# Performance work log

Hardware: AMD Instinct MI355X
Metric: run time of the kernel (lower is better)

## Reference

```python
import jax, jax.numpy as jnp
import numpy as np

D_MODEL = 256
NHEAD = 4
HEAD_DIM = D_MODEL // NHEAD
EPS = 1e-5


def layernorm(x, g, b):
    mu = jnp.mean(x, axis=-1, keepdims=True)
    var = jnp.mean((x - mu) ** 2, axis=-1, keepdims=True)
    return (x - mu) * jax.lax.rsqrt(var + EPS) * g + b


def setup_inputs() -> dict:
    key = jax.random.key(0)
    ks = jax.random.split(key, 16)
    bs, L, S = 2, 2048, 2048
    inp = {
        "x": jax.random.normal(ks[0], (bs, L, D_MODEL), jnp.float32),
        "source": jax.random.normal(ks[1], (bs, S, D_MODEL), jnp.float32),
        "x_pe": jax.random.normal(ks[2], (bs, L, D_MODEL), jnp.float32),
        "source_pe": jax.random.normal(ks[3], (bs, S, D_MODEL), jnp.float32),
        "x_mask": jax.random.randint(ks[4], (bs, L), 0, 2).astype(bool),
        "source_mask": jax.random.randint(ks[5], (bs, S), 0, 2).astype(bool),
        "compatibility": jax.random.uniform(ks[6], (bs, L, S), jnp.float32),
        # learned params (bias-free linears, two layernorms)
        "Wq": jax.random.normal(ks[7], (D_MODEL, D_MODEL), jnp.float32) * 0.05,
        "Wk": jax.random.normal(ks[8], (D_MODEL, D_MODEL), jnp.float32) * 0.05,
        "Wv": jax.random.normal(ks[9], (D_MODEL, D_MODEL), jnp.float32) * 0.05,
        "Wmerge": jax.random.normal(ks[10], (D_MODEL, D_MODEL), jnp.float32) * 0.05,
        "Wmlp1": jax.random.normal(ks[11], (2 * D_MODEL, 2 * D_MODEL), jnp.float32) * 0.05,
        "Wmlp2": jax.random.normal(ks[12], (2 * D_MODEL, D_MODEL), jnp.float32) * 0.05,
        "ln1_g": jnp.ones((D_MODEL,), jnp.float32),
        "ln1_b": jnp.zeros((D_MODEL,), jnp.float32),
        "ln2_g": jnp.ones((D_MODEL,), jnp.float32),
        "ln2_b": jnp.zeros((D_MODEL,), jnp.float32),
    }
    return inp


def reference(x, source, x_pe, source_pe, x_mask, source_mask, compatibility,
              Wq, Wk, Wv, Wmerge, Wmlp1, Wmlp2, ln1_g, ln1_b, ln2_g, ln2_b):
    bs = x.shape[0]
    # pe_type == 'sinusoidal': add PE before projections
    q_in = x + x_pe
    k_in = source + source_pe
    qw = (q_in @ Wq).reshape(bs, -1, NHEAD, HEAD_DIM)
    kw = (k_in @ Wk).reshape(bs, -1, NHEAD, HEAD_DIM)
    vw = (source @ Wv).reshape(bs, -1, NHEAD, HEAD_DIM)
    # scores (n, l, s, h)
    a = jnp.einsum('nlhd,nshd->nlsh', qw, kw)
    a = a * compatibility[..., None]
    mask = x_mask[:, :, None, None] & (~source_mask)[:, None, :, None]
    a = jnp.where(mask, -jnp.inf, a)
    a = a / jnp.sqrt(jnp.asarray(HEAD_DIM, a.dtype))
    a = jax.nn.softmax(a, axis=2)
    o = jnp.einsum('nlsh,nshd->nlhd', a, vw).reshape(bs, -1, D_MODEL)
    message = layernorm(o @ Wmerge, ln1_g, ln1_b)
    h = jnp.concatenate([x, message], axis=2)
    message = jax.nn.relu(h @ Wmlp1) @ Wmlp2
    message = layernorm(message, ln2_g, ln2_b)
    return x + message
```

## Files before the change

### kernel.cpp

```cpp
#include <hip/hip_runtime.h>
#include <cstddef>
#include <math.h>

#define D_MODEL 256
#define NHEAD 4
#define HEAD_DIM 64
#define BSZ 2
#define SEQ 2048
#define MROWS (BSZ * SEQ)
#define NSPLIT 4
#define SCHUNK (SEQ / NSPLIT)

typedef __attribute__((ext_vector_type(8))) short short8;
typedef __attribute__((ext_vector_type(4))) float f32x4;

__device__ __forceinline__ ushort f2bf_bits(float f) {
    union { float f; unsigned u; } c; c.f = f;
    unsigned u = c.u + 0x7fffu + ((c.u >> 16) & 1u);
    return (ushort)(u >> 16);
}
__device__ __forceinline__ float bf2f(ushort u) {
    union { unsigned u; float f; } c; c.u = (unsigned)u << 16;
    return c.f;
}

__global__ __launch_bounds__(256) void prepw_k(
    const float* __restrict__ Wq, const float* __restrict__ Wk,
    const float* __restrict__ Wv, const float* __restrict__ Wm,
    const float* __restrict__ W1, const float* __restrict__ W2,
    ushort* __restrict__ Wqt, ushort* __restrict__ Wkt,
    ushort* __restrict__ Wvt, ushort* __restrict__ Wmt,
    ushort* __restrict__ W1t, ushort* __restrict__ W2t)
{
    const int f0 = (blockIdx.x * 256 + threadIdx.x) * 16;
    const float* in; ushort* out; int Nd, ksh, r;
    if (f0 < 262144) {
        const int w = f0 >> 16; r = f0 & 65535; Nd = 256; ksh = 8;
        in  = (w == 0) ? Wq  : (w == 1) ? Wk  : (w == 2) ? Wv  : Wm;
        out = (w == 0) ? Wqt : (w == 1) ? Wkt : (w == 2) ? Wvt : Wmt;
    } else if (f0 < 524288) { r = f0 - 262144; Nd = 512; ksh = 9; in = W1; out = W1t; }
    else                    { r = f0 - 524288; Nd = 256; ksh = 9; in = W2; out = W2t; }
    const int n = r >> ksh, k = r & ((1 << ksh) - 1);
    ushort tmp[16];
#pragma unroll
    for (int i = 0; i < 16; i++) tmp[i] = f2bf_bits(in[(size_t)(k + i) * Nd + n]);
    *(uint4*)&out[r]     = *(uint4*)&tmp[0];
    *(uint4*)&out[r + 8] = *(uint4*)&tmp[8];
}

__global__ __launch_bounds__(256) void qkvp_k(
    const float* __restrict__ x, const float* __restrict__ xpe,
    const float* __restrict__ src, const float* __restrict__ spe,
    const ushort* __restrict__ Wqt, const ushort* __restrict__ Wkt,
    const ushort* __restrict__ Wvt,
    ushort* __restrict__ Qb, ushort* __restrict__ Kb, ushort* __restrict__ VtG)
{
    __shared__ __attribute__((aligned(16))) ushort As[16][264];

    const int z = blockIdx.y;
    const float* A1 = (z == 0) ? x : src;
    const float* A2 = (z == 0) ? xpe : (z == 1) ? spe : nullptr;
    const ushort* Bt = (z == 0) ? Wqt : (z == 1) ? Wkt : Wvt;
    ushort* out      = (z == 0) ? Qb  : (z == 1) ? Kb  : VtG;

    const int t = threadIdx.x, w = t >> 6, lane = t & 63;
    const int quad = lane >> 4, l16 = lane & 15;
    const int row0 = blockIdx.x * 16;

    {
        const int r = t >> 4, c0 = (t & 15) * 16;
        const size_t base = (size_t)(row0 + r) * 256 + c0;
        ushort tmp[16];
#pragma unroll
        for (int i = 0; i < 16; i += 4) {
            float4 a = *(const float4*)&A1[base + i];
            if (z < 2) {
                const float4 p = *(const float4*)&A2[base + i];
                a.x += p.x; a.y += p.y; a.z += p.z; a.w += p.w;
            }
            tmp[i] = f2bf_bits(a.x); tmp[i + 1] = f2bf_bits(a.y);
            tmp[i + 2] = f2bf_bits(a.z); tmp[i + 3] = f2bf_bits(a.w);
        }
        *(uint4*)&As[r][c0]     = *(uint4*)&tmp[0];
        *(uint4*)&As[r][c0 + 8] = *(uint4*)&tmp[8];
    }
    __syncthreads();

    f32x4 acc[4] = {};
#pragma unroll
    for (int k0 = 0; k0 < 256; k0 += 32) {
        const short8 aq = *(const short8*)&As[l16][k0 + quad * 8];
#pragma unroll
        for (int ct = 0; ct < 4; ct++) {
            const short8 bk =
                *(const short8*)&Bt[(size_t)(w * 64 + ct * 16 + l16) * 256 + k0 + quad * 8];
            acc[ct] = __builtin_amdgcn_mfma_f32_16x16x32_bf16(aq, bk, acc[ct], 0, 0, 0);
        }
    }

#pragma unroll
    for (int ct = 0; ct < 4; ct++) {
#pragma unroll
        for (int reg = 0; reg < 4; reg++) {
            const int grow = row0 + quad * 4 + reg;
            const int col  = w * 64 + ct * 16 + l16;
            const ushort v = f2bf_bits(acc[ct][reg]);
            if (z < 2) {
                out[(size_t)grow * 256 + col] = v;
            } else {
                const int b = grow >> 11, s = grow & 2047;
                out[((size_t)(b * 256 + col)) * 2048 + s] = v;
            }
        }
    }
}

__global__ __launch_bounds__(256, 4) void attn_k(
    const ushort* __restrict__ Q, const ushort* __restrict__ K,
    const ushort* __restrict__ Vt, const float* __restrict__ comp,
    const int* __restrict__ xmask, const int* __restrict__ smask,
    ushort* __restrict__ Opart, float* __restrict__ lbuf)
{
    __shared__ __attribute__((aligned(16))) ushort Ks[64][72];
    __shared__ __attribute__((aligned(16))) ushort Vs[64][72];
    __shared__ __attribute__((aligned(16))) ushort Ps[64][72];
    __shared__ int xms[64];
    __shared__ int sms[64];

    const int t    = threadIdx.x;
    const int w    = t >> 6;
    const int lane = t & 63;
    const int quad = lane >> 4;
    const int l16  = lane & 15;
    const int l0   = blockIdx.x * 64;
    const int h    = blockIdx.y;
    const int b    = blockIdx.z >> 2;
    const int sc   = blockIdx.z & 3;
    const int sbeg = sc * SCHUNK;

    const ushort* qp =
        &Q[((size_t)(b * SEQ + l0 + w * 16 + l16)) * D_MODEL + h * HEAD_DIM + quad * 8];
    const short8 q0 = *(const short8*)qp;
    const short8 q1 = *(const short8*)(qp + 32);

    if (t < 64) xms[t] = xmask[b * SEQ + l0 + t];

    const int rowbase = w * 16 + quad * 4;
    const int arow    = w * 16 + l16;
    const float* crow = comp + ((size_t)b * SEQ + l0 + rowbase) * SEQ;

    float lpart[4] = {0.f, 0.f, 0.f, 0.f};
    f32x4 oacc[4] = {};

    for (int s0 = sbeg; s0 < sbeg + SCHUNK; s0 += 64) {
        __syncthreads();
#pragma unroll
        for (int i = 0; i < 2; i++) {
            const int e = t + i * 256, r = e >> 3, cg = (e & 7) * 8;
            *(uint4*)&Ks[r][cg] =
                *(const uint4*)&K[((size_t)(b * SEQ + s0 + r)) * D_MODEL + h * HEAD_DIM + cg];
            *(uint4*)&Vs[r][cg] =
                *(const uint4*)&Vt[((size_t)(b * 256 + h * HEAD_DIM + r)) * SEQ + s0 + cg];
        }
        if (t < 64) sms[t] = smask[b * SEQ + s0 + t];

        float cv[16];
#pragma unroll
        for (int reg = 0; reg < 4; reg++)
#pragma unroll
            for (int ct = 0; ct < 4; ct++)
                cv[reg * 4 + ct] = crow[(size_t)reg * SEQ + s0 + ct * 16 + l16];

        __syncthreads();

        f32x4 sacc[4] = {};
#pragma unroll
        for (int ct = 0; ct < 4; ct++) {
            const short8 bk0 = *(const short8*)&Ks[ct * 16 + l16][quad * 8];
            sacc[ct] = __builtin_amdgcn_mfma_f32_16x16x32_bf16(q0, bk0, sacc[ct], 0, 0, 0);
        }
#pragma unroll
        for (int ct = 0; ct < 4; ct++) {
            const short8 bk1 = *(const short8*)&Ks[ct * 16 + l16][32 + quad * 8];
            sacc[ct] = __builtin_amdgcn_mfma_f32_16x16x32_bf16(q1, bk1, sacc[ct], 0, 0, 0);
        }

        const int sm0 = sms[l16], sm1 = sms[16 + l16], sm2 = sms[32 + l16], sm3 = sms[48 + l16];
#pragma unroll
        for (int reg = 0; reg < 4; reg++) {
            const bool xm = (xms[rowbase + reg] != 0);
            const float p0 = (xm && sm0 == 0) ? 0.f : __expf(sacc[0][reg] * cv[reg * 4 + 0] * 0.125f);
            const float p1 = (xm && sm1 == 0) ? 0.f : __expf(sacc[1][reg] * cv[reg * 4 + 1] * 0.125f);
            const float p2 = (xm && sm2 == 0) ? 0.f : __expf(sacc[2][reg] * cv[reg * 4 + 2] * 0.125f);
            const float p3 = (xm && sm3 == 0) ? 0.f : __expf(sacc[3][reg] * cv[reg * 4 + 3] * 0.125f);
            lpart[reg] += p0 + p1 + p2 + p3;
            Ps[rowbase + reg][l16]      = f2bf_bits(p0);
            Ps[rowbase + reg][16 + l16] = f2bf_bits(p1);
            Ps[rowbase + reg][32 + l16] = f2bf_bits(p2);
            Ps[rowbase + reg][48 + l16] = f2bf_bits(p3);
        }

#pragma unroll
        for (int kc = 0; kc < 64; kc += 32) {
            const short8 ap = *(const short8*)&Ps[arow][kc + quad * 8];
#pragma unroll
            for (int ct = 0; ct < 4; ct++) {
                const short8 bv = *(const short8*)&Vs[ct * 16 + l16][kc + quad * 8];
                oacc[ct] = __builtin_amdgcn_mfma_f32_16x16x32_bf16(ap, bv, oacc[ct], 0, 0, 0);
            }
        }
    }

#pragma unroll
    for (int off = 1; off < 16; off <<= 1)
#pragma unroll
        for (int reg = 0; reg < 4; reg++)
            lpart[reg] += __shfl_xor(lpart[reg], off, 64);

#pragma unroll
    for (int ct = 0; ct < 4; ct++)
#pragma unroll
        for (int reg = 0; reg < 4; reg++) {
            const int grow = b * SEQ + l0 + rowbase + reg;
            Opart[((size_t)sc * MROWS + grow) * D_MODEL + h * HEAD_DIM + ct * 16 + l16] =
                f2bf_bits(oacc[ct][reg]);
        }
    if (l16 == 0) {
#pragma unroll
        for (int reg = 0; reg < 4; reg++) {
            const int grow = b * SEQ + l0 + rowbase + reg;
            lbuf[((size_t)(sc * NHEAD + h)) * MROWS + grow] = lpart[reg];
        }
    }
}

__global__ __launch_bounds__(256) void tail_k(
    const ushort* __restrict__ Opart, const float* __restrict__ lbuf,
    const ushort* __restrict__ Wmt, const ushort* __restrict__ W1t,
    const ushort* __restrict__ W2t,
    const float* __restrict__ g1, const float* __restrict__ b1,
    const float* __restrict__ g2, const float* __restrict__ b2,
    const float* __restrict__ x, float* __restrict__ out)
{
    __shared__ __attribute__((aligned(16))) ushort As[16][264];
    __shared__ __attribute__((aligned(16))) ushort AH[16][520];
    __shared__ __attribute__((aligned(16))) ushort Hs[16][520];
    __shared__ float redS[4][16], redQ[4][16];

    const int t = threadIdx.x, w = t >> 6, lane = t & 63;
    const int quad = lane >> 4, l16 = lane & 15;
    const int row0 = blockIdx.x * 16;

    {
        const int r = t >> 4, cg = (t & 15) * 16;
        const int grow = row0 + r, h = (t & 15) >> 2;
        ushort tmp[16];
#pragma unroll
        for (int i = 0; i < 16; i += 4) {
            const float4 a = *(const float4*)&x[(size_t)grow * 256 + cg + i];
            tmp[i] = f2bf_bits(a.x); tmp[i + 1] = f2bf_bits(a.y);
            tmp[i + 2] = f2bf_bits(a.z); tmp[i + 3] = f2bf_bits(a.w);
        }
        *(uint4*)&AH[r][cg]     = *(uint4*)&tmp[0];
        *(uint4*)&AH[r][cg + 8] = *(uint4*)&tmp[8];

        float den = 0.f;
        float num[16] = {};
#pragma unroll
        for (int c = 0; c < NSPLIT; c++) {
            den += lbuf[((size_t)(c * NHEAD + h)) * MROWS + grow];
            const ushort* p = &Opart[((size_t)c * MROWS + grow) * D_MODEL + cg];
            uint4 u0 = *(const uint4*)p, u1 = *(const uint4*)(p + 8);
            const ushort* us0 = (const ushort*)&u0;
            const ushort* us1 = (const ushort*)&u1;
#pragma unroll
            for (int i = 0; i < 8; i++) { num[i] += bf2f(us0[i]); num[8 + i] += bf2f(us1[i]); }
        }
        const float inv = 1.f / den;
#pragma unroll
        for (int i = 0; i < 16; i++) tmp[i] = f2bf_bits(num[i] * inv);
        *(uint4*)&As[r][cg]     = *(uint4*)&tmp[0];
        *(uint4*)&As[r][cg + 8] = *(uint4*)&tmp[8];
    }
    __syncthreads();

    f32x4 macc[4] = {};
#pragma unroll
    for (int k0 = 0; k0 < 256; k0 += 32) {
        const short8 aq = *(const short8*)&As[l16][k0 + quad * 8];
#pragma unroll
        for (int ct = 0; ct < 4; ct++) {
            const short8 bk =
                *(const short8*)&Wmt[(size_t)(w * 64 + ct * 16 + l16) * 256 + k0 + quad * 8];
            macc[ct] = __builtin_amdgcn_mfma_f32_16x16x32_bf16(aq, bk, macc[ct], 0, 0, 0);
        }
    }

    {
        float ps[4] = {}, pq[4] = {};
#pragma unroll
        for (int ct = 0; ct < 4; ct++)
#pragma unroll
            for (int reg = 0; reg < 4; reg++) {
                ps[reg] += macc[ct][reg];
                pq[reg] += macc[ct][reg] * macc[ct][reg];
            }
#pragma unroll
        for (int off = 1; off < 16; off <<= 1)
#pragma unroll
            for (int reg = 0; reg < 4; reg++) {
                ps[reg] += __shfl_xor(ps[reg], off, 64);
                pq[reg] += __shfl_xor(pq[reg], off, 64);
            }
        if (l16 == 0)
#pragma unroll
            for (int reg = 0; reg < 4; reg++) {
                redS[w][quad * 4 + reg] = ps[reg];
                redQ[w][quad * 4 + reg] = pq[reg];
            }
    }
    __syncthreads();

#pragma unroll
    for (int reg = 0; reg < 4; reg++) {
        const int lrow = quad * 4 + reg;
        const float s  = redS[0][lrow] + redS[1][lrow] + redS[2][lrow] + redS[3][lrow];
        const float s2 = redQ[0][lrow] + redQ[1][lrow] + redQ[2][lrow] + redQ[3][lrow];
        const float mu  = s * (1.f / 256.f);
        const float var = s2 * (1.f / 256.f) - mu * mu;
        const float rr  = rsqrtf(var + 1e-5f);
#pragma unroll
        for (int ct = 0; ct < 4; ct++) {
            const int col = w * 64 + ct * 16 + l16;
            AH[lrow][256 + col] = f2bf_bits((macc[ct][reg] - mu) * rr * g1[col] + b1[col]);
        }
    }
    __syncthreads();

    {
        f32x4 hacc[8] = {};
#pragma unroll
        for (int k0 = 0; k0 < 512; k0 += 32) {
            const short8 aq = *(const short8*)&AH[l16][k0 + quad * 8];
#pragma unroll
            for (int ct = 0; ct < 8; ct++) {
                const short8 bk =
                    *(const short8*)&W1t[(size_t)(w * 128 + ct * 16 + l16) * 512 + k0 + quad * 8];
                hacc[ct] = __builtin_amdgcn_mfma_f32_16x16x32_bf16(aq, bk, hacc[ct], 0, 0, 0);
            }
        }
#pragma unroll
        for (int ct = 0; ct < 8; ct++)
#pragma unroll
            for (int reg = 0; reg < 4; reg++)
                Hs[quad * 4 + reg][w * 128 + ct * 16 + l16] =
                    f2bf_bits(fmaxf(hacc[ct][reg], 0.f));
    }
    __syncthreads();

    f32x4 acc[4] = {};
#pragma unroll
    for (int k0 = 0; k0 < 512; k0 += 32) {
        const short8 ap = *(const short8*)&Hs[l16][k0 + quad * 8];
#pragma unroll
        for (int ct = 0; ct < 4; ct++) {
            const short8 bk =
                *(const short8*)&W2t[(size_t)(w * 64 + ct * 16 + l16) * 512 + k0 + quad * 8];
            acc[ct] = __builtin_amdgcn_mfma_f32_16x16x32_bf16(ap, bk, acc[ct], 0, 0, 0);
        }
    }

    {
        float ps[4] = {}, pq[4] = {};
#pragma unroll
        for (int ct = 0; ct < 4; ct++)
#pragma unroll
            for (int reg = 0; reg < 4; reg++) {
                ps[reg] += acc[ct][reg];
                pq[reg] += acc[ct][reg] * acc[ct][reg];
            }
#pragma unroll
        for (int off = 1; off < 16; off <<= 1)
#pragma unroll
            for (int reg = 0; reg < 4; reg++) {
                ps[reg] += __shfl_xor(ps[reg], off, 64);
                pq[reg] += __shfl_xor(pq[reg], off, 64);
            }
        if (l16 == 0)
#pragma unroll
            for (int reg = 0; reg < 4; reg++) {
                redS[w][quad * 4 + reg] = ps[reg];
                redQ[w][quad * 4 + reg] = pq[reg];
            }
    }
    __syncthreads();

#pragma unroll
    for (int reg = 0; reg < 4; reg++) {
        const int lrow = quad * 4 + reg;
        const float s  = redS[0][lrow] + redS[1][lrow] + redS[2][lrow] + redS[3][lrow];
        const float s2 = redQ[0][lrow] + redQ[1][lrow] + redQ[2][lrow] + redQ[3][lrow];
        const float mu  = s * (1.f / 256.f);
        const float var = s2 * (1.f / 256.f) - mu * mu;
        const float rr  = rsqrtf(var + 1e-5f);
#pragma unroll
        for (int ct = 0; ct < 4; ct++) {
            const int col = w * 64 + ct * 16 + l16;
            const size_t idx = (size_t)(row0 + lrow) * 256 + col;
            out[idx] = (acc[ct][reg] - mu) * rr * g2[col] + b2[col] + x[idx];
        }
    }
}

extern "C" void kernel_launch(void* const* d_in, const int* in_sizes, int n_in,
                              void* d_out, int out_size, void* d_ws, size_t ws_size,
                              hipStream_t stream)
{
    (void)in_sizes; (void)n_in; (void)out_size; (void)ws_size;
    const float* x      = (const float*)d_in[0];
    const float* source = (const float*)d_in[1];
    const float* x_pe   = (const float*)d_in[2];
    const float* s_pe   = (const float*)d_in[3];
    const int*   x_mask = (const int*)d_in[4];
    const int*   s_mask = (const int*)d_in[5];
    const float* comp   = (const float*)d_in[6];
    const float* Wq     = (const float*)d_in[7];
    const float* Wk     = (const float*)d_in[8];
    const float* Wv     = (const float*)d_in[9];
    const float* Wmerge = (const float*)d_in[10];
    const float* Wmlp1  = (const float*)d_in[11];
    const float* Wmlp2  = (const float*)d_in[12];
    const float* ln1_g  = (const float*)d_in[13];
    const float* ln1_b  = (const float*)d_in[14];
    const float* ln2_g  = (const float*)d_in[15];
    const float* ln2_b  = (const float*)d_in[16];
    float* out = (float*)d_out;
    char*  ws  = (char*)d_ws;

    const size_t MB = 1024 * 1024;
    ushort* Qb    = (ushort*)(ws + 0 * MB);
    ushort* Kb    = (ushort*)(ws + 2 * MB);
    ushort* VtG   = (ushort*)(ws + 4 * MB);
    ushort* Opart = (ushort*)(ws + 6 * MB);
    float*  lbuf  = (float*)(ws + 14 * MB);
    ushort* Wqt   = (ushort*)(ws + 15 * MB);
    ushort* Wkt   = (ushort*)(ws + 15 * MB + 128 * 1024);
    ushort* Wvt   = (ushort*)(ws + 15 * MB + 256 * 1024);
    ushort* Wmt   = (ushort*)(ws + 15 * MB + 384 * 1024);
    ushort* W1t   = (ushort*)(ws + 15 * MB + 512 * 1024);
    ushort* W2t   = (ushort*)(ws + 16 * MB);

    prepw_k<<<160, 256, 0, stream>>>(Wq, Wk, Wv, Wmerge, Wmlp1, Wmlp2,
                                     Wqt, Wkt, Wvt, Wmt, W1t, W2t);

    qkvp_k<<<dim3(MROWS / 16, 3), 256, 0, stream>>>(
        x, x_pe, source, s_pe, Wqt, Wkt, Wvt, Qb, Kb, VtG);

    attn_k<<<dim3(SEQ / 64, NHEAD, BSZ * NSPLIT), 256, 0, stream>>>(
        Qb, Kb, VtG, comp, x_mask, s_mask, Opart, lbuf);

    tail_k<<<MROWS / 16, 256, 0, stream>>>(
        Opart, lbuf, Wmt, W1t, W2t, ln1_g, ln1_b, ln2_g, ln2_b, x, out);
}
```

Measured before the change: 185.9 us.

## Fuse four kernels into one persistent kernel with grid-wide barriers

Merges the weight-prep, QKV projection, attention and tail kernels into a single launch of 1024 blocks that step through the phases, separated by atomic-counter grid barriers. Shared memory is a union of the per-phase layouts. The aim is to remove per-kernel launch overhead and the gaps between dependent launches. In exchange it adds a memset launch, spin-wait barriers that idle many blocks in the phases that use fewer blocks, and a deadlock risk if all 1024 blocks cannot be resident at once (256 CUs × 4 blocks).

Result: slower. 689.9 us (+271.1%).

```diff
diff --git a/kernel.cpp b/kernel.cpp
--- a/kernel.cpp
+++ b/kernel.cpp
@@ -10,6 +10,7 @@
 #define MROWS (BSZ * SEQ)
 #define NSPLIT 4
 #define SCHUNK (SEQ / NSPLIT)
+#define GRIDN 1024
 
 typedef __attribute__((ext_vector_type(8))) short short8;
 typedef __attribute__((ext_vector_type(4))) float f32x4;
@@ -24,390 +25,398 @@
     return c.f;
 }
 
-__global__ __launch_bounds__(256) void prepw_k(
-    const float* __restrict__ Wq, const float* __restrict__ Wk,
-    const float* __restrict__ Wv, const float* __restrict__ Wm,
-    const float* __restrict__ W1, const float* __restrict__ W2,
-    ushort* __restrict__ Wqt, ushort* __restrict__ Wkt,
-    ushort* __restrict__ Wvt, ushort* __restrict__ Wmt,
-    ushort* __restrict__ W1t, ushort* __restrict__ W2t)
-{
-    const int f0 = (blockIdx.x * 256 + threadIdx.x) * 16;
-    const float* in; ushort* out; int Nd, ksh, r;
-    if (f0 < 262144) {
-        const int w = f0 >> 16; r = f0 & 65535; Nd = 256; ksh = 8;
-        in  = (w == 0) ? Wq  : (w == 1) ? Wk  : (w == 2) ? Wv  : Wm;
-        out = (w == 0) ? Wqt : (w == 1) ? Wkt : (w == 2) ? Wvt : Wmt;
-    } else if (f0 < 524288) { r = f0 - 262144; Nd = 512; ksh = 9; in = W1; out = W1t; }
-    else                    { r = f0 - 524288; Nd = 256; ksh = 9; in = W2; out = W2t; }
-    const int n = r >> ksh, k = r & ((1 << ksh) - 1);
-    ushort tmp[16];
-#pragma unroll
-    for (int i = 0; i < 16; i++) tmp[i] = f2bf_bits(in[(size_t)(k + i) * Nd + n]);
-    *(uint4*)&out[r]     = *(uint4*)&tmp[0];
-    *(uint4*)&out[r + 8] = *(uint4*)&tmp[8];
-}
-
-__global__ __launch_bounds__(256) void qkvp_k(
-    const float* __restrict__ x, const float* __restrict__ xpe,
-    const float* __restrict__ src, const float* __restrict__ spe,
-    const ushort* __restrict__ Wqt, const ushort* __restrict__ Wkt,
-    const ushort* __restrict__ Wvt,
-    ushort* __restrict__ Qb, ushort* __restrict__ Kb, ushort* __restrict__ VtG)
-{
-    __shared__ __attribute__((aligned(16))) ushort As[16][264];
-
-    const int z = blockIdx.y;
-    const float* A1 = (z == 0) ? x : src;
-    const float* A2 = (z == 0) ? xpe : (z == 1) ? spe : nullptr;
-    const ushort* Bt = (z == 0) ? Wqt : (z == 1) ? Wkt : Wvt;
-    ushort* out      = (z == 0) ? Qb  : (z == 1) ? Kb  : VtG;
-
-    const int t = threadIdx.x, w = t >> 6, lane = t & 63;
-    const int quad = lane >> 4, l16 = lane & 15;
-    const int row0 = blockIdx.x * 16;
-
-    {
-        const int r = t >> 4, c0 = (t & 15) * 16;
-        const size_t base = (size_t)(row0 + r) * 256 + c0;
-        ushort tmp[16];
-#pragma unroll
-        for (int i = 0; i < 16; i += 4) {
-            float4 a = *(const float4*)&A1[base + i];
-            if (z < 2) {
-                const float4 p = *(const float4*)&A2[base + i];
-                a.x += p.x; a.y += p.y; a.z += p.z; a.w += p.w;
-            }
-            tmp[i] = f2bf_bits(a.x); tmp[i + 1] = f2bf_bits(a.y);
-            tmp[i + 2] = f2bf_bits(a.z); tmp[i + 3] = f2bf_bits(a.w);
-        }
-        *(uint4*)&As[r][c0]     = *(uint4*)&tmp[0];
-        *(uint4*)&As[r][c0 + 8] = *(uint4*)&tmp[8];
+struct Params {
+    const float *x, *xpe, *src, *spe;
+    const int *xmk, *smk;
+    const float *comp;
+    const float *Wq, *Wk, *Wv, *Wm, *W1, *W2;
+    const float *g1, *b1, *g2, *b2;
+    float *out;
+    ushort *Qb, *Kb, *VtG, *Opart;
+    float *lbuf;
+    ushort *Wqt, *Wkt, *Wvt, *Wmt, *W1t, *W2t;
+    int *bar;
+};
+
+__device__ __forceinline__ void gbar(int* ctr) {
+    __syncthreads();
+    __threadfence();
+    if (threadIdx.x == 0) {
+        atomicAdd(ctr, 1);
+        while (atomicAdd(ctr, 0) < GRIDN) __builtin_amdgcn_s_sleep(2);
     }
     __syncthreads();
-
-    f32x4 acc[4] = {};
-#pragma unroll
-    for (int k0 = 0; k0 < 256; k0 += 32) {
-        const short8 aq = *(const short8*)&As[l16][k0 + quad * 8];
+}
+
+struct SAttn {
+    ushort Ks[64][72];
+    ushort Vs[64][72];
+    ushort Ps[64][72];
+    int xms[64];
+    int sms[64];
+};
+struct STail {
+    ushort AH[16][520];
+    ushort Hs[16][520];
+    float redS[4][16];
+    float redQ[4][16];
+};
+struct SQkv { ushort As[16][264]; };
+union SMem { SAttn a; STail t; SQkv q; };
+
+__global__ __launch_bounds__(256, 4) void fused_k(Params p)
+{
+    __shared__ __attribute__((aligned(16))) SMem sm;
+
+    const int bid = blockIdx.x, t = threadIdx.x;
+    const int w = t >> 6, lane = t & 63;
+    const int quad = lane >> 4, l16 = lane & 15;
+
+    if (bid < 160) {
+        const int f0 = (bid * 256 + t) * 16;
+        const float* in; ushort* out; int Nd, ksh, r;
+        if (f0 < 262144) {
+            const int ws = f0 >> 16; r = f0 & 65535; Nd = 256; ksh = 8;
+            in  = (ws == 0) ? p.Wq  : (ws == 1) ? p.Wk  : (ws == 2) ? p.Wv  : p.Wm;
+            out = (ws == 0) ? p.Wqt : (ws == 1) ? p.Wkt : (ws == 2) ? p.Wvt : p.Wmt;
+        } else if (f0 < 524288) { r = f0 - 262144; Nd = 512; ksh = 9; in = p.W1; out = p.W1t; }
+        else                    { r = f0 - 524288; Nd = 256; ksh = 9; in = p.W2; out = p.W2t; }
+        const int n = r >> ksh, k = r & ((1 << ksh) - 1);
+        ushort tmp[16];
+#pragma unroll
+        for (int i = 0; i < 16; i++) tmp[i] = f2bf_bits(in[(size_t)(k + i) * Nd + n]);
+        *(uint4*)&out[r]     = *(uint4*)&tmp[0];
+        *(uint4*)&out[r + 8] = *(uint4*)&tmp[8];
+    }
+    gbar(&p.bar[0]);
+
+    if (bid < 768) {
+        const int z = bid >> 8;
+        const int row0 = (bid & 255) * 16;
+        const float* A1 = (z == 0) ? p.x : p.src;
+        const float* A2 = (z == 0) ? p.xpe : (z == 1) ? p.spe : nullptr;
+        const ushort* Bt = (z == 0) ? p.Wqt : (z == 1) ? p.Wkt : p.Wvt;
+        ushort* out      = (z == 0) ? p.Qb  : (z == 1) ? p.Kb  : p.VtG;
+
+        {
+            const int r = t >> 4, c0 = (t & 15) * 16;
+            const size_t base = (size_t)(row0 + r) * 256 + c0;
+            ushort tmp[16];
+#pragma unroll
+            for (int i = 0; i < 16; i += 4) {
+                float4 a = *(const float4*)&A1[base + i];
+                if (z < 2) {
+                    const float4 pe = *(const float4*)&A2[base + i];
+                    a.x += pe.x; a.y += pe.y; a.z += pe.z; a.w += pe.w;
+                }
+                tmp[i] = f2bf_bits(a.x); tmp[i + 1] = f2bf_bits(a.y);
+                tmp[i + 2] = f2bf_bits(a.z); tmp[i + 3] = f2bf_bits(a.w);
+            }
+            *(uint4*)&sm.q.As[r][c0]     = *(uint4*)&tmp[0];
+            *(uint4*)&sm.q.As[r][c0 + 8] = *(uint4*)&tmp[8];
+        }
+        __syncthreads();
+
+        f32x4 acc[4] = {};
+#pragma unroll
+        for (int k0 = 0; k0 < 256; k0 += 32) {
+            const short8 aq = *(const short8*)&sm.q.As[l16][k0 + quad * 8];
+#pragma unroll
+            for (int ct = 0; ct < 4; ct++) {
+                const short8 bk =
+                    *(const short8*)&Bt[(size_t)(w * 64 + ct * 16 + l16) * 256 + k0 + quad * 8];
+                acc[ct] = __builtin_amdgcn_mfma_f32_16x16x32_bf16(aq, bk, acc[ct], 0, 0, 0);
+            }
+        }
+
 #pragma unroll
         for (int ct = 0; ct < 4; ct++) {
-            const short8 bk =
-                *(const short8*)&Bt[(size_t)(w * 64 + ct * 16 + l16) * 256 + k0 + quad * 8];
-            acc[ct] = __builtin_amdgcn_mfma_f32_16x16x32_bf16(aq, bk, acc[ct], 0, 0, 0);
+#pragma unroll
+            for (int reg = 0; reg < 4; reg++) {
+                const int grow = row0 + quad * 4 + reg;
+                const int col  = w * 64 + ct * 16 + l16;
+                const ushort v = f2bf_bits(acc[ct][reg]);
+                if (z < 2) {
+                    out[(size_t)grow * 256 + col] = v;
+                } else {
+                    const int b = grow >> 11, s = grow & 2047;
+                    out[((size_t)(b * 256 + col)) * 2048 + s] = v;
+                }
+            }
         }
     }
-
-#pragma unroll
-    for (int ct = 0; ct < 4; ct++) {
+    gbar(&p.bar[1]);
+
+    {
+        const int l0 = (bid & 31) * 64;
+        const int h  = (bid >> 5) & 3;
+        const int zz = bid >> 7;
+        const int b  = zz >> 2;
+        const int sc = zz & 3;
+        const int sbeg = sc * SCHUNK;
+
+        const ushort* qp =
+            &p.Qb[((size_t)(b * SEQ + l0 + w * 16 + l16)) * D_MODEL + h * HEAD_DIM + quad * 8];
+        const short8 q0 = *(const short8*)qp;
+        const short8 q1 = *(const short8*)(qp + 32);
+
+        if (t < 64) sm.a.xms[t] = p.xmk[b * SEQ + l0 + t];
+
+        const int rowbase = w * 16 + quad * 4;
+        const int arow    = w * 16 + l16;
+        const float* crow = p.comp + ((size_t)b * SEQ + l0 + rowbase) * SEQ;
+
+        float lpart[4] = {0.f, 0.f, 0.f, 0.f};
+        f32x4 oacc[4] = {};
+
+        for (int s0 = sbeg; s0 < sbeg + SCHUNK; s0 += 64) {
+            __syncthreads();
+#pragma unroll
+            for (int i = 0; i < 2; i++) {
+                const int e = t + i * 256, r = e >> 3, cgc = (e & 7) * 8;
+                *(uint4*)&sm.a.Ks[r][cgc] =
+                    *(const uint4*)&p.Kb[((size_t)(b * SEQ + s0 + r)) * D_MODEL + h * HEAD_DIM + cgc];
+                *(uint4*)&sm.a.Vs[r][cgc] =
+                    *(const uint4*)&p.VtG[((size_t)(b * 256 + h * HEAD_DIM + r)) * SEQ + s0 + cgc];
+            }
+            if (t < 64) sm.a.sms[t] = p.smk[b * SEQ + s0 + t];
+
+            float cv[16];
+#pragma unroll
+            for (int reg = 0; reg < 4; reg++)
+#pragma unroll
+                for (int ct = 0; ct < 4; ct++)
+                    cv[reg * 4 + ct] = crow[(size_t)reg * SEQ + s0 + ct * 16 + l16];
+
+            __syncthreads();
+
+            f32x4 sacc[4] = {};
+#pragma unroll
+            for (int ct = 0; ct < 4; ct++) {
+                const short8 bk0 = *(const short8*)&sm.a.Ks[ct * 16 + l16][quad * 8];
+                sacc[ct] = __builtin_amdgcn_mfma_f32_16x16x32_bf16(q0, bk0, sacc[ct], 0, 0, 0);
+            }
+#pragma unroll
+            for (int ct = 0; ct < 4; ct++) {
+                const short8 bk1 = *(const short8*)&sm.a.Ks[ct * 16 + l16][32 + quad * 8];
+                sacc[ct] = __builtin_amdgcn_mfma_f32_16x16x32_bf16(q1, bk1, sacc[ct], 0, 0, 0);
+            }
+
+            const int s0m = sm.a.sms[l16], s1m = sm.a.sms[16 + l16];
+            const int s2m = sm.a.sms[32 + l16], s3m = sm.a.sms[48 + l16];
+#pragma unroll
+            for (int reg = 0; reg < 4; reg++) {
+                const bool xm = (sm.a.xms[rowbase + reg] != 0);
+                const float p0 = (xm && s0m == 0) ? 0.f : __expf(sacc[0][reg] * cv[reg * 4 + 0] * 0.125f);
+                const float p1 = (xm && s1m == 0) ? 0.f : __expf(sacc[1][reg] * cv[reg * 4 + 1] * 0.125f);
+                const float p2 = (xm && s2m == 0) ? 0.f : __expf(sacc[2][reg] * cv[reg * 4 + 2] * 0.125f);
+                const float p3 = (xm && s3m == 0) ? 0.f : __expf(sacc[3][reg] * cv[reg * 4 + 3] * 0.125f);
+                lpart[reg] += p0 + p1 + p2 + p3;
+                sm.a.Ps[rowbase + reg][l16]      = f2bf_bits(p0);
+                sm.a.Ps[rowbase + reg][16 + l16] = f2bf_bits(p1);
+                sm.a.Ps[rowbase + reg][32 + l16] = f2bf_bits(p2);
+                sm.a.Ps[rowbase + reg][48 + l16] = f2bf_bits(p3);
+            }
+
+#pragma unroll
+            for (int kc = 0; kc < 64; kc += 32) {
+                const short8 ap = *(const short8*)&sm.a.Ps[arow][kc + quad * 8];
+#pragma unroll
+                for (int ct = 0; ct < 4; ct++) {
+                    const short8 bv = *(const short8*)&sm.a.Vs[ct * 16 + l16][kc + quad * 8];
+                    oacc[ct] = __builtin_amdgcn_mfma_f32_16x16x32_bf16(ap, bv, oacc[ct], 0, 0, 0);
+                }
+            }
+        }
+
+#pragma unroll
+        for (int off = 1; off < 16; off <<= 1)
+#pragma unroll
+            for (int reg = 0; reg < 4; reg++)
+                lpart[reg] += __shfl_xor(lpart[reg], off, 64);
+
+#pragma unroll
+        for (int ct = 0; ct < 4; ct++)
+#pragma unroll
+            for (int reg = 0; reg < 4; reg++) {
+                const int grow = b * SEQ + l0 + rowbase + reg;
+                p.Opart[((size_t)sc * MROWS + grow) * D_MODEL + h * HEAD_DIM + ct * 16 + l16] =
+                    f2bf_bits(oacc[ct][reg]);
+            }
+        if (l16 == 0) {
+#pragma unroll
+            for (int reg = 0; reg < 4; reg++) {
+                const int grow = b * SEQ + l0 + rowbase + reg;
+                p.lbuf[((size_t)(sc * NHEAD + h)) * MROWS + grow] = lpart[reg];
+            }
+        }
+    }
+    gbar(&p.bar[2]);
+
+    if (bid < 256) {
+        const int row0 = bid * 16;
+        ushort* AsP = &sm.t.Hs[0][0];
+
+        {
+            const int r = t >> 4, cgc = (t & 15) * 16;
+            const int grow = row0 + r, h = (t & 15) >> 2;
+            ushort tmp[16];
+#pragma unroll
+            for (int i = 0; i < 16; i += 4) {
+                const float4 a = *(const float4*)&p.x[(size_t)grow * 256 + cgc + i];
+                tmp[i] = f2bf_bits(a.x); tmp[i + 1] = f2bf_bits(a.y);
+                tmp[i + 2] = f2bf_bits(a.z); tmp[i + 3] = f2bf_bits(a.w);
+            }
+            *(uint4*)&sm.t.AH[r][cgc]     = *(uint4*)&tmp[0];
+            *(uint4*)&sm.t.AH[r][cgc + 8] = *(uint4*)&tmp[8];
+
+            float den = 0.f;
+            float num[16] = {};
+#pragma unroll
+            for (int c = 0; c < NSPLIT; c++) {
+                den += p.lbuf[((size_t)(c * NHEAD + h)) * MROWS + grow];
+                const ushort* pp = &p.Opart[((size_t)c * MROWS + grow) * D_MODEL + cgc];
+                uint4 u0 = *(const uint4*)pp, u1 = *(const uint4*)(pp + 8);
+                const ushort* us0 = (const ushort*)&u0;
+                const ushort* us1 = (const ushort*)&u1;
+#pragma unroll
+                for (int i = 0; i < 8; i++) { num[i] += bf2f(us0[i]); num[8 + i] += bf2f(us1[i]); }
+            }
+            const float inv = 1.f / den;
+#pragma unroll
+            for (int i = 0; i < 16; i++) tmp[i] = f2bf_bits(num[i] * inv);
+            *(uint4*)&AsP[r * 264 + cgc]     = *(uint4*)&tmp[0];
+            *(uint4*)&AsP[r * 264 + cgc + 8] = *(uint4*)&tmp[8];
+        }
+        __syncthreads();
+
+        f32x4 macc[4] = {};
+#pragma unroll
+        for (int k0 = 0; k0 < 256; k0 += 32) {
+            const short8 aq = *(const short8*)&AsP[l16 * 264 + k0 + quad * 8];
+#pragma unroll
+            for (int ct = 0; ct < 4; ct++) {
+                const short8 bk =
+                    *(const short8*)&p.Wmt[(size_t)(w * 64 + ct * 16 + l16) * 256 + k0 + quad * 8];
+                macc[ct] = __builtin_amdgcn_mfma_f32_16x16x32_bf16(aq, bk, macc[ct], 0, 0, 0);
+            }
+        }
+
+        {
+            float ps[4] = {}, pq[4] = {};
+#pragma unroll
+            for (int ct = 0; ct < 4; ct++)
+#pragma unroll
+                for (int reg = 0; reg < 4; reg++) {
+                    ps[reg] += macc[ct][reg];
+                    pq[reg] += macc[ct][reg] * macc[ct][reg];
+                }
+#pragma unroll
+            for (int off = 1; off < 16; off <<= 1)
+#pragma unroll
+                for (int reg = 0; reg < 4; reg++) {
+                    ps[reg] += __shfl_xor(ps[reg], off, 64);
+                    pq[reg] += __shfl_xor(pq[reg], off, 64);
+                }
+            if (l16 == 0)
+#pragma unroll
+                for (int reg = 0; reg < 4; reg++) {
+                    sm.t.redS[w][quad * 4 + reg] = ps[reg];
+                    sm.t.redQ[w][quad * 4 + reg] = pq[reg];
+                }
+        }
+        __syncthreads();
+
 #pragma unroll
         for (int reg = 0; reg < 4; reg++) {
-            const int grow = row0 + quad * 4 + reg;
-            const int col  = w * 64 + ct * 16 + l16;
-            const ushort v = f2bf_bits(acc[ct][reg]);
-            if (z < 2) {
-                out[(size_t)grow * 256 + col] = v;
-            } else {
-                const int b = grow >> 11, s = grow & 2047;
-                out[((size_t)(b * 256 + col)) * 2048 + s] = v;
-            }
-        }
-    }
-}
-
-__global__ __launch_bounds__(256, 4) void attn_k(
-    const ushort* __restrict__ Q, const ushort* __restrict__ K,
-    const ushort* __restrict__ Vt, const float* __restrict__ comp,
-    const int* __restrict__ xmask, const int* __restrict__ smask,
-    ushort* __restrict__ Opart, float* __restrict__ lbuf)
-{
-    __shared__ __attribute__((aligned(16))) ushort Ks[64][72];
-    __shared__ __attribute__((aligned(16))) ushort Vs[64][72];
-    __shared__ __attribute__((aligned(16))) ushort Ps[64][72];
-    __shared__ int xms[64];
-    __shared__ int sms[64];
-
-    const int t    = threadIdx.x;
-    const int w    = t >> 6;
-    const int lane = t & 63;
-    const int quad = lane >> 4;
-    const int l16  = lane & 15;
-    const int l0   = blockIdx.x * 64;
-    const int h    = blockIdx.y;
-    const int b    = blockIdx.z >> 2;
-    const int sc   = blockIdx.z & 3;
-    const int sbeg = sc * SCHUNK;
-
-    const ushort* qp =
-        &Q[((size_t)(b * SEQ + l0 + w * 16 + l16)) * D_MODEL + h * HEAD_DIM + quad * 8];
-    const short8 q0 = *(const short8*)qp;
-    const short8 q1 = *(const short8*)(qp + 32);
-
-    if (t < 64) xms[t] = xmask[b * SEQ + l0 + t];
-
-    const int rowbase = w * 16 + quad * 4;
-    const int arow    = w * 16 + l16;
-    const float* crow = comp + ((size_t)b * SEQ + l0 + rowbase) * SEQ;
-
-    float lpart[4] = {0.f, 0.f, 0.f, 0.f};
-    f32x4 oacc[4] = {};
-
-    for (int s0 = sbeg; s0 < sbeg + SCHUNK; s0 += 64) {
-        __syncthreads();
-#pragma unroll
-        for (int i = 0; i < 2; i++) {
-            const int e = t + i * 256, r = e >> 3, cg = (e & 7) * 8;
-            *(uint4*)&Ks[r][cg] =
-                *(const uint4*)&K[((size_t)(b * SEQ + s0 + r)) * D_MODEL + h * HEAD_DIM + cg];
-            *(uint4*)&Vs[r][cg] =
-                *(const uint4*)&Vt[((size_t)(b * 256 + h * HEAD_DIM + r)) * SEQ + s0 + cg];
-        }
-        if (t < 64) sms[t] = smask[b * SEQ + s0 + t];
-
-        float cv[16];
-#pragma unroll
-        for (int reg = 0; reg < 4; reg++)
+            const int lrow = quad * 4 + reg;
+            const float s  = sm.t.redS[0][lrow] + sm.t.redS[1][lrow] + sm.t.redS[2][lrow] + sm.t.redS[3][lrow];
+            const float s2 = sm.t.redQ[0][lrow] + sm.t.redQ[1][lrow] + sm.t.redQ[2][lrow] + sm.t.redQ[3][lrow];
+            const float mu  = s * (1.f / 256.f);
+            const float var = s2 * (1.f / 256.f) - mu * mu;
+            const float rr  = rsqrtf(var + 1e-5f);
+#pragma unroll
+            for (int ct = 0; ct < 4; ct++) {
+                const int col = w * 64 + ct * 16 + l16;
+                sm.t.AH[lrow][256 + col] =
+                    f2bf_bits((macc[ct][reg] - mu) * rr * p.g1[col] + p.b1[col]);
+            }
+        }
+        __syncthreads();
+
+        {
+            f32x4 hacc[8] = {};
+#pragma unroll
+            for (int k0 = 0; k0 < 512; k0 += 32) {
+                const short8 aq = *(const short8*)&sm.t.AH[l16][k0 + quad * 8];
+#pragma unroll
+                for (int ct = 0; ct < 8; ct++) {
+                    const short8 bk =
+                        *(const short8*)&p.W1t[(size_t)(w * 128 + ct * 16 + l16) * 512 + k0 + quad * 8];
+                    hacc[ct] = __builtin_amdgcn_mfma_f32_16x16x32_bf16(aq, bk, hacc[ct], 0, 0, 0);
+                }
+            }
+            __syncthreads();
+#pragma unroll
+            for (int ct = 0; ct < 8; ct++)
+#pragma unroll
+                for (int reg = 0; reg < 4; reg++)
+                    sm.t.Hs[quad * 4 + reg][w * 128 + ct * 16 + l16] =
+                        f2bf_bits(fmaxf(hacc[ct][reg], 0.f));
+        }
+        __syncthreads();
+
+        f32x4 acc[4] = {};
+#pragma unroll
+        for (int k0 = 0; k0 < 512; k0 += 32) {
+            const short8 ap = *(const short8*)&sm.t.Hs[l16][k0 + quad * 8];
+#pragma unroll
+            for (int ct = 0; ct < 4; ct++) {
+                const short8 bk =
+                    *(const short8*)&p.W2t[(size_t)(w * 64 + ct * 16 + l16) * 512 + k0 + quad * 8];
+                acc[ct] = __builtin_amdgcn_mfma_f32_16x16x32_bf16(ap, bk, acc[ct], 0, 0, 0);
+            }
+        }
+
+        {
+            float ps[4] = {}, pq[4] = {};
 #pragma unroll
             for (int ct = 0; ct < 4; ct++)
-                cv[reg * 4 + ct] = crow[(size_t)reg * SEQ + s0 + ct * 16 + l16];
-
-        __syncthreads();
-
-        f32x4 sacc[4] = {};
-#pragma unroll
-        for (int ct = 0; ct < 4; ct++) {
-            const short8 bk0 = *(const short8*)&Ks[ct * 16 + l16][quad * 8];
-            sacc[ct] = __builtin_amdgcn_mfma_f32_16x16x32_bf16(q0, bk0, sacc[ct], 0, 0, 0);
-        }
-#pragma unroll
-        for (int ct = 0; ct < 4; ct++) {
-            const short8 bk1 = *(const short8*)&Ks[ct * 16 + l16][32 + quad * 8];
-            sacc[ct] = __builtin_amdgcn_mfma_f32_16x16x32_bf16(q1, bk1, sacc[ct], 0, 0, 0);
-        }
-
-        const int sm0 = sms[l16], sm1 = sms[16 + l16], sm2 = sms[32 + l16], sm3 = sms[48 + l16];
+#pragma unroll
+                for (int reg = 0; reg < 4; reg++) {
+                    ps[reg] += acc[ct][reg];
+                    pq[reg] += acc[ct][reg] * acc[ct][reg];
+                }
+#pragma unroll
+            for (int off = 1; off < 16; off <<= 1)
+#pragma unroll
+                for (int reg = 0; reg < 4; reg++) {
+                    ps[reg] += __shfl_xor(ps[reg], off, 64);
+                    pq[reg] += __shfl_xor(pq[reg], off, 64);
+                }
+            if (l16 == 0)
+#pragma unroll
+                for (int reg = 0; reg < 4; reg++) {
+                    sm.t.redS[w][quad * 4 + reg] = ps[reg];
+                    sm.t.redQ[w][quad * 4 + reg] = pq[reg];
+                }
+        }
+        __syncthreads();
+
 #pragma unroll
         for (int reg = 0; reg < 4; reg++) {
-            const bool xm = (xms[rowbase + reg] != 0);
-            const float p0 = (xm && sm0 == 0) ? 0.f : __expf(sacc[0][reg] * cv[reg * 4 + 0] * 0.125f);
-            const float p1 = (xm && sm1 == 0) ? 0.f : __expf(sacc[1][reg] * cv[reg * 4 + 1] * 0.125f);
-            const float p2 = (xm && sm2 == 0) ? 0.f : __expf(sacc[2][reg] * cv[reg * 4 + 2] * 0.125f);
-            const float p3 = (xm && sm3 == 0) ? 0.f : __expf(sacc[3][reg] * cv[reg * 4 + 3] * 0.125f);
-            lpart[reg] += p0 + p1 + p2 + p3;
-            Ps[rowbase + reg][l16]      = f2bf_bits(p0);
-            Ps[rowbase + reg][16 + l16] = f2bf_bits(p1);
-            Ps[rowbase + reg][32 + l16] = f2bf_bits(p2);
-            Ps[rowbase + reg][48 + l16] = f2bf_bits(p3);
-        }
-
-#pragma unroll
-        for (int kc = 0; kc < 64; kc += 32) {
-            const short8 ap = *(const short8*)&Ps[arow][kc + quad * 8];
-#pragma unroll
-            for (int ct = 0; ct < 4; ct++) {
-                const short8 bv = *(const short8*)&Vs[ct * 16 + l16][kc + quad * 8];
-                oacc[ct] = __builtin_amdgcn_mfma_f32_16x16x32_bf16(ap, bv, oacc[ct], 0, 0, 0);
-            }
-        }
-    }
-
-#pragma unroll
-    for (int off = 1; off < 16; off <<= 1)
-#pragma unroll
-        for (int reg = 0; reg < 4; reg++)
-            lpart[reg] += __shfl_xor(lpart[reg], off, 64);
-
-#pragma unroll
-    for (int ct = 0; ct < 4; ct++)
-#pragma unroll
-        for (int reg = 0; reg < 4; reg++) {
-            const int grow = b * SEQ + l0 + rowbase + reg;
-            Opart[((size_t)sc * MROWS + grow) * D_MODEL + h * HEAD_DIM + ct * 16 + l16] =
-                f2bf_bits(oacc[ct][reg]);
-        }
-    if (l16 == 0) {
-#pragma unroll
-        for (int reg = 0; reg < 4; reg++) {
-            const int grow = b * SEQ + l0 + rowbase + reg;
-            lbuf[((size_t)(sc * NHEAD + h)) * MROWS + grow] = lpart[reg];
-        }
-    }
-}
-
-__global__ __launch_bounds__(256) void tail_k(
-    const ushort* __restrict__ Opart, const float* __restrict__ lbuf,
-    const ushort* __restrict__ Wmt, const ushort* __restrict__ W1t,
-    const ushort* __restrict__ W2t,
-    const float* __restrict__ g1, const float* __restrict__ b1,
-    const float* __restrict__ g2, const float* __restrict__ b2,
-    const float* __restrict__ x, float* __restrict__ out)
-{
-    __shared__ __attribute__((aligned(16))) ushort As[16][264];
-    __shared__ __attribute__((aligned(16))) ushort AH[16][520];
-    __shared__ __attribute__((aligned(16))) ushort Hs[16][520];
-    __shared__ float redS[4][16], redQ[4][16];
-
-    const int t = threadIdx.x, w = t >> 6, lane = t & 63;
-    const int quad = lane >> 4, l16 = lane & 15;
-    const int row0 = blockIdx.x * 16;
-
-    {
-        const int r = t >> 4, cg = (t & 15) * 16;
-        const int grow = row0 + r, h = (t & 15) >> 2;
-        ushort tmp[16];
-#pragma unroll
-        for (int i = 0; i < 16; i += 4) {
-            const float4 a = *(const float4*)&x[(size_t)grow * 256 + cg + i];
-            tmp[i] = f2bf_bits(a.x); tmp[i + 1] = f2bf_bits(a.y);
-            tmp[i + 2] = f2bf_bits(a.z); tmp[i + 3] = f2bf_bits(a.w);
-        }
-        *(uint4*)&AH[r][cg]     = *(uint4*)&tmp[0];
-        *(uint4*)&AH[r][cg + 8] = *(uint4*)&tmp[8];
-
-        float den = 0.f;
-        float num[16] = {};
-#pragma unroll
-        for (int c = 0; c < NSPLIT; c++) {
-            den += lbuf[((size_t)(c * NHEAD + h)) * MROWS + grow];
-            const ushort* p = &Opart[((size_t)c * MROWS + grow) * D_MODEL + cg];
-            uint4 u0 = *(const uint4*)p, u1 = *(const uint4*)(p + 8);
-            const ushort* us0 = (const ushort*)&u0;
-            const ushort* us1 = (const ushort*)&u1;
-#pragma unroll
-            for (int i = 0; i < 8; i++) { num[i] += bf2f(us0[i]); num[8 + i] += bf2f(us1[i]); }
-        }
-        const float inv = 1.f / den;
-#pragma unroll
-        for (int i = 0; i < 16; i++) tmp[i] = f2bf_bits(num[i] * inv);
-        *(uint4*)&As[r][cg]     = *(uint4*)&tmp[0];
-        *(uint4*)&As[r][cg + 8] = *(uint4*)&tmp[8];
-    }
-    __syncthreads();
-
-    f32x4 macc[4] = {};
-#pragma unroll
-    for (int k0 = 0; k0 < 256; k0 += 32) {
-        const short8 aq = *(const short8*)&As[l16][k0 + quad * 8];
-#pragma unroll
-        for (int ct = 0; ct < 4; ct++) {
-            const short8 bk =
-                *(const short8*)&Wmt[(size_t)(w * 64 + ct * 16 + l16) * 256 + k0 + quad * 8];
-            macc[ct] = __builtin_amdgcn_mfma_f32_16x16x32_bf16(aq, bk, macc[ct], 0, 0, 0);
-        }
-    }
-
-    {
-        float ps[4] = {}, pq[4] = {};
-#pragma unroll
-        for (int ct = 0; ct < 4; ct++)
-#pragma unroll
-            for (int reg = 0; reg < 4; reg++) {
-                ps[reg] += macc[ct][reg];
-                pq[reg] += macc[ct][reg] * macc[ct][reg];
-            }
-#pragma unroll
-        for (int off = 1; off < 16; off <<= 1)
-#pragma unroll
-            for (int reg = 0; reg < 4; reg++) {
-                ps[reg] += __shfl_xor(ps[reg], off, 64);
-                pq[reg] += __shfl_xor(pq[reg], off, 64);
-            }
-        if (l16 == 0)
-#pragma unroll
-            for (int reg = 0; reg < 4; reg++) {
-                redS[w][quad * 4 + reg] = ps[reg];
-                redQ[w][quad * 4 + reg] = pq[reg];
-            }
-    }
-    __syncthreads();
-
-#pragma unroll
-    for (int reg = 0; reg < 4; reg++) {
-        const int lrow = quad * 4 + reg;
-        const float s  = redS[0][lrow] + redS[1][lrow] + redS[2][lrow] + redS[3][lrow];
-        const float s2 = redQ[0][lrow] + redQ[1][lrow] + redQ[2][lrow] + redQ[3][lrow];
-        const float mu  = s * (1.f / 256.f);
-        const float var = s2 * (1.f / 256.f) - mu * mu;
-        const float rr  = rsqrtf(var + 1e-5f);
-#pragma unroll
-        for (int ct = 0; ct < 4; ct++) {
-            const int col = w * 64 + ct * 16 + l16;
-            AH[lrow][256 + col] = f2bf_bits((macc[ct][reg] - mu) * rr * g1[col] + b1[col]);
-        }
-    }
-    __syncthreads();
-
-    {
-        f32x4 hacc[8] = {};
-#pragma unroll
-        for (int k0 = 0; k0 < 512; k0 += 32) {
-            const short8 aq = *(const short8*)&AH[l16][k0 + quad * 8];
-#pragma unroll
-            for (int ct = 0; ct < 8; ct++) {
-                const short8 bk =
-                    *(const short8*)&W1t[(size_t)(w * 128 + ct * 16 + l16) * 512 + k0 + quad * 8];
-                hacc[ct] = __builtin_amdgcn_mfma_f32_16x16x32_bf16(aq, bk, hacc[ct], 0, 0, 0);
-            }
-        }
-#pragma unroll
-        for (int ct = 0; ct < 8; ct++)
-#pragma unroll
-            for (int reg = 0; reg < 4; reg++)
-                Hs[quad * 4 + reg][w * 128 + ct * 16 + l16] =
-                    f2bf_bits(fmaxf(hacc[ct][reg], 0.f));
-    }
-    __syncthreads();
-
-    f32x4 acc[4] = {};
-#pragma unroll
-    for (int k0 = 0; k0 < 512; k0 += 32) {
-        const short8 ap = *(const short8*)&Hs[l16][k0 + quad * 8];
-#pragma unroll
-        for (int ct = 0; ct < 4; ct++) {
-            const short8 bk =
-                *(const short8*)&W2t[(size_t)(w * 64 + ct * 16 + l16) * 512 + k0 + quad * 8];
-            acc[ct] = __builtin_amdgcn_mfma_f32_16x16x32_bf16(ap, bk, acc[ct], 0, 0, 0);
-        }
-    }
-
-    {
-        float ps[4] = {}, pq[4] = {};
-#pragma unroll
-        for (int ct = 0; ct < 4; ct++)
-#pragma unroll
-            for (int reg = 0; reg < 4; reg++) {
-                ps[reg] += acc[ct][reg];
-                pq[reg] += acc[ct][reg] * acc[ct][reg];
-            }
-#pragma unroll
-        for (int off = 1; off < 16; off <<= 1)
-#pragma unroll
-            for (int reg = 0; reg < 4; reg++) {
-                ps[reg] += __shfl_xor(ps[reg], off, 64);
-                pq[reg] += __shfl_xor(pq[reg], off, 64);
-            }
-        if (l16 == 0)
-#pragma unroll
-            for (int reg = 0; reg < 4; reg++) {
-                redS[w][quad * 4 + reg] = ps[reg];
-                redQ[w][quad * 4 + reg] = pq[reg];
-            }
-    }
-    __syncthreads();
-
-#pragma unroll
-    for (int reg = 0; reg < 4; reg++) {
-        const int lrow = quad * 4 + reg;
-        const float s  = redS[0][lrow] + redS[1][lrow] + redS[2][lrow] + redS[3][lrow];
-        const float s2 = redQ[0][lrow] + redQ[1][lrow] + redQ[2][lrow] + redQ[3][lrow];
-        const float mu  = s * (1.f / 256.f);
-        const float var = s2 * (1.f / 256.f) - mu * mu;
-        const float rr  = rsqrtf(var + 1e-5f);
-#pragma unroll
-        for (int ct = 0; ct < 4; ct++) {
-            const int col = w * 64 + ct * 16 + l16;
-            const size_t idx = (size_t)(row0 + lrow) * 256 + col;
-            out[idx] = (acc[ct][reg] - mu) * rr * g2[col] + b2[col] + x[idx];
+            const int lrow = quad * 4 + reg;
+            const float s  = sm.t.redS[0][lrow] + sm.t.redS[1][lrow] + sm.t.redS[2][lrow] + sm.t.redS[3][lrow];
+            const float s2 = sm.t.redQ[0][lrow] + sm.t.redQ[1][lrow] + sm.t.redQ[2][lrow] + sm.t.redQ[3][lrow];
+            const float mu  = s * (1.f / 256.f);
+            const float var = s2 * (1.f / 256.f) - mu * mu;
+            const float rr  = rsqrtf(var + 1e-5f);
+#pragma unroll
+            for (int ct = 0; ct < 4; ct++) {
+                const int col = w * 64 + ct * 16 + l16;
+                const size_t idx = (size_t)(row0 + lrow) * 256 + col;
+                p.out[idx] = (acc[ct][reg] - mu) * rr * p.g2[col] + p.b2[col] + p.x[idx];
+            }
         }
     }
 }
@@ -417,48 +426,42 @@
                               hipStream_t stream)
 {
     (void)in_sizes; (void)n_in; (void)out_size; (void)ws_size;
-    const float* x      = (const float*)d_in[0];
-    const float* source = (const float*)d_in[1];
-    const float* x_pe   = (const float*)d_in[2];
-    const float* s_pe   = (const float*)d_in[3];
-    const int*   x_mask = (const int*)d_in[4];
-    const int*   s_mask = (const int*)d_in[5];
-    const float* comp   = (const float*)d_in[6];
-    const float* Wq     = (const float*)d_in[7];
-    const float* Wk     = (const float*)d_in[8];
-    const float* Wv     = (const float*)d_in[9];
-    const float* Wmerge = (const float*)d_in[10];
-    const float* Wmlp1  = (const float*)d_in[11];
-    const float* Wmlp2  = (const float*)d_in[12];
-    const float* ln1_g  = (const float*)d_in[13];
-    const float* ln1_b  = (const float*)d_in[14];
-    const float* ln2_g  = (const float*)d_in[15];
-    const float* ln2_b  = (const float*)d_in[16];
-    float* out = (float*)d_out;
-    char*  ws  = (char*)d_ws;
-
+    char* ws = (char*)d_ws;
     const size_t MB = 1024 * 1024;
-    ushort* Qb    = (ushort*)(ws + 0 * MB);
-    ushort* Kb    = (ushort*)(ws + 2 * MB);
-    ushort* VtG   = (ushort*)(ws + 4 * MB);
-    ushort* Opart = (ushort*)(ws + 6 * MB);
-    float*  lbuf  = (float*)(ws + 14 * MB);
-    ushort* Wqt   = (ushort*)(ws + 15 * MB);
-    ushort* Wkt   = (ushort*)(ws + 15 * MB + 128 * 1024);
-    ushort* Wvt   = (ushort*)(ws + 15 * MB + 256 * 1024);
-    ushort* Wmt   = (ushort*)(ws + 15 * MB + 384 * 1024);
-    ushort* W1t   = (ushort*)(ws + 15 * MB + 512 * 1024);
-    ushort* W2t   = (ushort*)(ws + 16 * MB);
-
-    prepw_k<<<160, 256, 0, stream>>>(Wq, Wk, Wv, Wmerge, Wmlp1, Wmlp2,
-                                     Wqt, Wkt, Wvt, Wmt, W1t, W2t);
-
-    qkvp_k<<<dim3(MROWS / 16, 3), 256, 0, stream>>>(
-        x, x_pe, source, s_pe, Wqt, Wkt, Wvt, Qb, Kb, VtG);
-
-    attn_k<<<dim3(SEQ / 64, NHEAD, BSZ * NSPLIT), 256, 0, stream>>>(
-        Qb, Kb, VtG, comp, x_mask, s_mask, Opart, lbuf);
-
-    tail_k<<<MROWS / 16, 256, 0, stream>>>(
-        Opart, lbuf, Wmt, W1t, W2t, ln1_g, ln1_b, ln2_g, ln2_b, x, out);
+
+    Params p;
+    p.x    = (const float*)d_in[0];
+    p.src  = (const float*)d_in[1];
+    p.xpe  = (const float*)d_in[2];
+    p.spe  = (const float*)d_in[3];
+    p.xmk  = (const int*)d_in[4];
+    p.smk  = (const int*)d_in[5];
+    p.comp = (const float*)d_in[6];
+    p.Wq   = (const float*)d_in[7];
+    p.Wk   = (const float*)d_in[8];
+    p.Wv   = (const float*)d_in[9];
+    p.Wm   = (const float*)d_in[10];
+    p.W1   = (const float*)d_in[11];
+    p.W2   = (const float*)d_in[12];
+    p.g1   = (const float*)d_in[13];
+    p.b1   = (const float*)d_in[14];
+    p.g2   = (const float*)d_in[15];
+    p.b2   = (const float*)d_in[16];
+    p.out  = (float*)d_out;
+
+    p.Qb    = (ushort*)(ws + 0 * MB);
+    p.Kb    = (ushort*)(ws + 2 * MB);
+    p.VtG   = (ushort*)(ws + 4 * MB);
+    p.Opart = (ushort*)(ws + 6 * MB);
+    p.lbuf  = (float*)(ws + 14 * MB);
+    p.Wqt   = (ushort*)(ws + 15 * MB);
+    p.Wkt   = (ushort*)(ws + 15 * MB + 128 * 1024);
+    p.Wvt   = (ushort*)(ws + 15 * MB + 256 * 1024);
+    p.Wmt   = (ushort*)(ws + 15 * MB + 384 * 1024);
+    p.W1t   = (ushort*)(ws + 15 * MB + 512 * 1024);
+    p.W2t   = (ushort*)(ws + 16 * MB);
+    p.bar   = (int*)(ws + 17 * MB);
+
+    hipMemsetAsync(p.bar, 0, 64, stream);
+    fused_k<<<GRIDN, 256, 0, stream>>>(p);
 }
```
